# Optimization experiments

Measured on AMD Instinct MI355X. Metric: run time of the kernel, lower is better.

The kernel has to match this reference:

```python
import jax, jax.numpy as jnp
import numpy as np

BN_EPS = 1e-5
LN_EPS = 1e-5


def setup_inputs() -> dict:
    key = jax.random.key(0)
    ks = jax.random.split(key, 8)
    B, D, T = 16, 96, 512  # batch, enc_in (channels), d_model (time/feature)
    H = 2 * T
    residual = jax.random.normal(ks[0], (B, D, T), dtype=jnp.float32)
    # BatchNorm1d(enc_in) affine params
    bn_gamma = jnp.ones((D,), dtype=jnp.float32)
    bn_beta = jnp.zeros((D,), dtype=jnp.float32)
    # LayerNorm(d_model) affine params
    ln_gamma = jnp.ones((T,), dtype=jnp.float32)
    ln_beta = jnp.zeros((T,), dtype=jnp.float32)
    # MLP: Linear(T, 2T) -> GELU -> Linear(2T, T)
    W1 = jax.random.normal(ks[1], (T, H), dtype=jnp.float32) / np.float32(np.sqrt(T))
    b1 = jnp.zeros((H,), dtype=jnp.float32)
    W2 = jax.random.normal(ks[2], (H, T), dtype=jnp.float32) / np.float32(np.sqrt(H))
    b2 = jnp.zeros((T,), dtype=jnp.float32)
    return {"residual": residual, "bn_gamma": bn_gamma, "bn_beta": bn_beta,
            "ln_gamma": ln_gamma, "ln_beta": ln_beta,
            "W1": W1, "b1": b1, "W2": W2, "b2": b2}


def _var_cor_attention(x):
    # x: [B, D, T]; queries = keys = values = x
    B, D, T = x.shape
    f = jnp.fft.rfft(x, axis=-1)                       # [B, D, F]
    # pairwise spectral product q_i * conj(k_j): [B, D, D, F]
    res = f[:, :, None, :] * jnp.conj(f[:, None, :, :])
    corr = jnp.fft.irfft(res, axis=-1).mean(axis=-1)   # [B, D, D]
    scale = np.float32(1.0 / np.sqrt(T))
    corr = jax.nn.softmax(corr * scale, axis=-1)
    V = jnp.einsum('bsd,bde->bse', corr, x)            # [B, D, T]
    return V


def reference(residual, bn_gamma, bn_beta, ln_gamma, ln_beta, W1, b1, W2, b2):
    # attention + residual
    x = _var_cor_attention(residual) + residual        # [B, D, T]
    # BatchNorm1d over channel dim D: stats over (B, T), biased variance
    mu = x.mean(axis=(0, 2), keepdims=True)
    var = ((x - mu) ** 2).mean(axis=(0, 2), keepdims=True)
    x = (x - mu) * jax.lax.rsqrt(var + BN_EPS)
    x = x * bn_gamma[None, :, None] + bn_beta[None, :, None]
    # MLP (exact GELU, torch default) + residual
    h = jax.nn.gelu(jnp.einsum('bdt,th->bdh', x, W1) + b1, approximate=False)
    y = jnp.einsum('bdh,ht->bdt', h, W2) + b2 + x
    # LayerNorm over last dim T
    mu2 = y.mean(axis=-1, keepdims=True)
    var2 = ((y - mu2) ** 2).mean(axis=-1, keepdims=True)
    y = (y - mu2) * jax.lax.rsqrt(var2 + LN_EPS)
    return y * ln_gamma + ln_beta
```

## Files before the change

kernel.cpp:

```cpp
#include <hip/hip_runtime.h>
#include <math.h>
#include <stdint.h>

#define BB 16
#define DD 96
#define TT 512
#define HH 1024
#define NROW (BB*DD)
#define KT2 (HH/32)

typedef __attribute__((ext_vector_type(4))) float floatx4;
typedef __attribute__((ext_vector_type(8))) short short8;

#define WSOFF_X     0u
#define WSOFF_A     3145728u
#define WSOFF_HFRAG WSOFF_A
#define WSOFF_W1BF  6291456u
#define WSOFF_W2BF  7340032u
#define WSOFF_PS    8388608u
#define WSOFF_PS2   8437760u
#define WSOFF_SCSH  8486912u

__device__ __forceinline__ uint16_t f2bf(float v) {
    uint32_t u = __float_as_uint(v);
    uint32_t r = 0x7fffu + ((u >> 16) & 1u);
    return (uint16_t)((u + r) >> 16);
}

__global__ __launch_bounds__(256) void k_pre(const float* __restrict__ residual,
                                             const float* __restrict__ W1,
                                             const float* __restrict__ W2,
                                             float* __restrict__ A,
                                             uint16_t* __restrict__ w1bf,
                                             uint16_t* __restrict__ w2bf) {
    __shared__ float sl[DD];
    const int bid = blockIdx.x;
    const int tid = threadIdx.x;
    const int wave = tid >> 6;
    const int lane = tid & 63;
    const int q = lane >> 4, l15 = lane & 15;

    if (bid < BB) {
        #pragma unroll
        for (int rr = 0; rr < 24; ++rr) {
            int i = wave*24 + rr;
            const float* p = residual + ((size_t)bid*DD + i)*TT;
            float acc = 0.f;
            #pragma unroll
            for (int u = 0; u < TT/64; ++u) acc += p[lane + u*64];
            #pragma unroll
            for (int o = 32; o > 0; o >>= 1) acc += __shfl_down(acc, o, 64);
            if (lane == 0) sl[i] = acc;
        }
        __syncthreads();
        if (tid < DD) {
            const float c = 1.0f / (512.0f * 22.627416997969522f);
            float si = sl[tid] * c;
            float m = -1e30f;
            for (int j = 0; j < DD; ++j) m = fmaxf(m, si * sl[j]);
            float sum = 0.f;
            for (int j = 0; j < DD; ++j) sum += __expf(si * sl[j] - m);
            float inv = 1.0f / sum;
            float* Ao = A + ((size_t)bid*DD + tid)*DD;
            for (int j = 0; j < DD; ++j) Ao[j] = __expf(si * sl[j] - m) * inv;
        }
    } else {
        int wgid = (bid - BB)*4 + wave;
        const int nw = (512 - BB)*4;
        for (int u = wgid; u < 2048; u += nw) {
            const float* W; uint16_t* ob; int KT, N, b;
            if (u < 1024) { W = W1; ob = w1bf; KT = 16; N = 1024; b = u; }
            else          { W = W2; ob = w2bf; KT = 32; N = 512;  b = u - 1024; }
            int tile_n = b / KT, tile_k = b % KT;
            const float* src = W + (size_t)(tile_k*32 + q*8)*N + tile_n*16 + l15;
            uint16_t tmp[8];
            #pragma unroll
            for (int j = 0; j < 8; ++j) tmp[j] = f2bf(src[(size_t)j*N]);
            uint16_t* dst = ob + ((size_t)b*64 + lane)*8;
            *reinterpret_cast<ushort4*>(dst)     = *reinterpret_cast<ushort4*>(&tmp[0]);
            *reinterpret_cast<ushort4*>(dst + 4) = *reinterpret_cast<ushort4*>(&tmp[4]);
        }
    }
}

__global__ __launch_bounds__(256) void k_attn(const float* __restrict__ residual,
                                              const float* __restrict__ A,
                                              float* __restrict__ x,
                                              float* __restrict__ ps,
                                              float* __restrict__ ps2) {
    __shared__ float rlds[DD*64];
    const int u = blockIdx.x;
    const int b = u >> 5, chunk = (u >> 2) & 7, ig = u & 3;
    const int tid = threadIdx.x;
    const int wave = tid >> 6;
    const int lane = tid & 63;

    const float4* rb4 = reinterpret_cast<const float4*>(residual + (size_t)b*DD*TT);
    float4* rl4 = reinterpret_cast<float4*>(rlds);
    #pragma unroll
    for (int s = 0; s < 6; ++s) {
        int idx = tid + s*256;
        int i = idx >> 4, t4 = idx & 15;
        rl4[idx] = rb4[(size_t)i*(TT/4) + chunk*16 + t4];
    }
    __syncthreads();

    int i0 = ig*24 + wave*6;
    const float* Ab = A + ((size_t)b*DD + i0)*DD;
    float acc[6];
    #pragma unroll
    for (int rr = 0; rr < 6; ++rr) acc[rr] = rlds[(i0+rr)*64 + lane];
    #pragma unroll 4
    for (int j4 = 0; j4 < DD/4; ++j4) {
        float4 a[6];
        #pragma unroll
        for (int rr = 0; rr < 6; ++rr)
            a[rr] = *reinterpret_cast<const float4*>(Ab + rr*DD + j4*4);
        float rv[4];
        #pragma unroll
        for (int uu = 0; uu < 4; ++uu) rv[uu] = rlds[(j4*4+uu)*64 + lane];
        #pragma unroll
        for (int rr = 0; rr < 6; ++rr) {
            acc[rr] = fmaf(a[rr].x, rv[0], acc[rr]);
            acc[rr] = fmaf(a[rr].y, rv[1], acc[rr]);
            acc[rr] = fmaf(a[rr].z, rv[2], acc[rr]);
            acc[rr] = fmaf(a[rr].w, rv[3], acc[rr]);
        }
    }
    #pragma unroll
    for (int rr = 0; rr < 6; ++rr) {
        float v = acc[rr];
        x[((size_t)b*DD + i0 + rr)*TT + chunk*64 + lane] = v;
        float s1 = v, s2 = v*v;
        #pragma unroll
        for (int o = 32; o > 0; o >>= 1) {
            s1 += __shfl_down(s1, o, 64);
            s2 += __shfl_down(s2, o, 64);
        }
        if (lane == 0) {
            int d = i0 + rr;
            ps [d*128 + b*8 + chunk] = s1;
            ps2[d*128 + b*8 + chunk] = s2;
        }
    }
}

__global__ __launch_bounds__(256) void k_gemm1(const float* __restrict__ x,
                                               const float* __restrict__ ps,
                                               const float* __restrict__ ps2,
                                               const float* __restrict__ bng,
                                               const float* __restrict__ bnb,
                                               const uint16_t* __restrict__ w1bf,
                                               const float* __restrict__ b1,
                                               uint16_t* __restrict__ hfrag,
                                               float* __restrict__ scsh) {
    __shared__ __align__(16) char SM[27136];
    uint16_t* fragA = (uint16_t*)SM;
    uint16_t* cs    = (uint16_t*)(SM + 16384);
    float*    fin   = (float*)(SM + 24832);
    float*    scs   = (float*)(SM + 26368);
    const int bid = blockIdx.x;
    const int tid = threadIdx.x;
    const int wave = tid >> 6;
    const int lane = tid & 63;
    const int q = lane >> 4, l15 = lane & 15;

    if (tid < 192) {
        int d = tid >> 1, h = tid & 1;
        const float4* p1 = reinterpret_cast<const float4*>(ps  + d*128 + h*64);
        const float4* p2 = reinterpret_cast<const float4*>(ps2 + d*128 + h*64);
        float a1 = 0.f, a2 = 0.f;
        #pragma unroll
        for (int j = 0; j < 16; ++j) {
            float4 v = p1[j]; a1 += v.x+v.y+v.z+v.w;
            float4 w = p2[j]; a2 += w.x+w.y+w.z+w.w;
        }
        fin[tid*2]   = a1;
        fin[tid*2+1] = a2;
    }
    __syncthreads();
    if (tid < DD) {
        float s1 = fin[tid*4]   + fin[tid*4+2];
        float s2 = fin[tid*4+1] + fin[tid*4+3];
        const float invn = 1.0f / (float)(BB*TT);
        float mu  = s1 * invn;
        float var = s2 * invn - mu*mu;
        float rs  = rsqrtf(var + 1e-5f);
        float scv = rs * bng[tid];
        float shv = bnb[tid] - mu*scv;
        scs[tid]      = scv;
        scs[DD + tid] = shv;
        if (bid == 0) { scsh[tid] = scv; scsh[DD + tid] = shv; }
    }
    __syncthreads();

    const int mtile = bid >> 2, nq = bid & 3;
    #pragma unroll
    for (int r4 = 0; r4 < 4; ++r4) {
        int pi = tid + r4*256;
        int kk = pi >> 6, pl = pi & 63;
        int pq = pl >> 4, pr = pl & 15;
        int row = mtile*16 + pr;
        int d = row % DD;
        float scv = scs[d], shv = scs[DD + d];
        const float* xp = x + (size_t)row*TT + kk*32 + pq*8;
        float4 v0 = *reinterpret_cast<const float4*>(xp);
        float4 v1 = *reinterpret_cast<const float4*>(xp + 4);
        ushort4 o0, o1;
        o0.x = f2bf(v0.x*scv + shv); o0.y = f2bf(v0.y*scv + shv);
        o0.z = f2bf(v0.z*scv + shv); o0.w = f2bf(v0.w*scv + shv);
        o1.x = f2bf(v1.x*scv + shv); o1.y = f2bf(v1.y*scv + shv);
        o1.z = f2bf(v1.z*scv + shv); o1.w = f2bf(v1.w*scv + shv);
        uint16_t* fp = fragA + ((size_t)kk*64 + pl)*8;
        *reinterpret_cast<ushort4*>(fp)     = o0;
        *reinterpret_cast<ushort4*>(fp + 4) = o1;
    }
    __syncthreads();

    int n0 = nq*256 + wave*64;
    floatx4 acc4[4] = {};
    #pragma unroll
    for (int kk = 0; kk < 16; ++kk) {
        short8 a = *reinterpret_cast<const short8*>(fragA + (kk*64 + lane)*8);
        #pragma unroll
        for (int nf = 0; nf < 4; ++nf) {
            int ct = (n0 >> 4) + nf;
            short8 bfr = *reinterpret_cast<const short8*>(
                w1bf + ((size_t)(ct*16 + kk)*64 + lane)*8);
            acc4[nf] = __builtin_amdgcn_mfma_f32_16x16x32_bf16(a, bfr, acc4[nf], 0, 0, 0);
        }
    }
    #pragma unroll
    for (int nf = 0; nf < 4; ++nf) {
        int coll = wave*64 + nf*16 + l15;
        float bias = b1[nq*256 + coll];
        #pragma unroll
        for (int r = 0; r < 4; ++r) {
            float v = acc4[nf][r] + bias;
            float gl = 0.5f * v * (1.0f + erff(v * 0.7071067811865475f));
            cs[(q*4 + r)*264 + coll] = f2bf(gl);
        }
    }
    __syncthreads();
    #pragma unroll
    for (int cc = 0; cc < 2; ++cc) {
        int c = wave*2 + cc;
        const uint4* srcp = reinterpret_cast<const uint4*>(cs + l15*264 + c*32 + q*8);
        size_t chunk = (size_t)mtile*KT2 + nq*8 + c;
        reinterpret_cast<uint4*>(hfrag)[chunk*64 + lane] = *srcp;
    }
}

__global__ __launch_bounds__(256) void k_gemm2(const uint16_t* __restrict__ hfrag,
                                               const uint16_t* __restrict__ w2bf,
                                               const float* __restrict__ b2,
                                               const float* __restrict__ x,
                                               const float* __restrict__ scsh,
                                               const float* __restrict__ lng,
                                               const float* __restrict__ lnb,
                                               float* __restrict__ out) {
    __shared__ float lnred[128];
    const int mtile = blockIdx.x;
    const int tid = threadIdx.x;
    const int wave = tid >> 6;
    const int lane = tid & 63;
    const int q = lane >> 4, l15 = lane & 15;
    const int m0 = mtile*16;
    const int n0 = wave*128;

    floatx4 acc[8] = {};
    const uint16_t* ap = hfrag + ((size_t)mtile*KT2*64 + lane)*8;
    #pragma unroll
    for (int kk = 0; kk < 32; ++kk) {
        short8 a = *reinterpret_cast<const short8*>(ap + kk*512);
        #pragma unroll
        for (int nf = 0; nf < 8; ++nf) {
            int ct = (n0 >> 4) + nf;
            short8 bfr = *reinterpret_cast<const short8*>(
                w2bf + ((size_t)(ct*32 + kk)*64 + lane)*8);
            acc[nf] = __builtin_amdgcn_mfma_f32_16x16x32_bf16(a, bfr, acc[nf], 0, 0, 0);
        }
    }
    float s_pt[4]  = {0.f,0.f,0.f,0.f};
    float s2_pt[4] = {0.f,0.f,0.f,0.f};
    #pragma unroll
    for (int r = 0; r < 4; ++r) {
        int row = m0 + q*4 + r;
        int d = row % DD;
        float scv = scsh[d], shv = scsh[DD + d];
        #pragma unroll
        for (int nf = 0; nf < 8; ++nf) {
            int col = n0 + nf*16 + l15;
            float v = acc[nf][r] + b2[col] + x[(size_t)row*TT + col]*scv + shv;
            acc[nf][r] = v;
            s_pt[r]  += v;
            s2_pt[r] += v*v;
        }
    }
    #pragma unroll
    for (int o = 1; o < 16; o <<= 1) {
        #pragma unroll
        for (int r = 0; r < 4; ++r) {
            s_pt[r]  += __shfl_xor(s_pt[r],  o, 64);
            s2_pt[r] += __shfl_xor(s2_pt[r], o, 64);
        }
    }
    if (l15 == 0) {
        #pragma unroll
        for (int r = 0; r < 4; ++r) {
            lnred[(wave*16 + q*4 + r)*2]     = s_pt[r];
            lnred[(wave*16 + q*4 + r)*2 + 1] = s2_pt[r];
        }
    }
    __syncthreads();
    #pragma unroll
    for (int r = 0; r < 4; ++r) {
        int rloc = q*4 + r;
        float s1 = lnred[rloc*2]   + lnred[(16+rloc)*2]   + lnred[(32+rloc)*2]   + lnred[(48+rloc)*2];
        float s2 = lnred[rloc*2+1] + lnred[(16+rloc)*2+1] + lnred[(32+rloc)*2+1] + lnred[(48+rloc)*2+1];
        const float invT = 1.0f / (float)TT;
        float mu  = s1 * invT;
        float var = s2 * invT - mu*mu;
        float rs  = rsqrtf(var + 1e-5f);
        int row = m0 + rloc;
        #pragma unroll
        for (int nf = 0; nf < 8; ++nf) {
            int col = n0 + nf*16 + l15;
            out[(size_t)row*TT + col] = (acc[nf][r] - mu)*rs*lng[col] + lnb[col];
        }
    }
}

extern "C" void kernel_launch(void* const* d_in, const int* in_sizes, int n_in,
                              void* d_out, int out_size, void* d_ws, size_t ws_size,
                              hipStream_t stream) {
    (void)in_sizes; (void)n_in; (void)out_size; (void)ws_size;
    const float* residual = (const float*)d_in[0];
    const float* bng = (const float*)d_in[1];
    const float* bnb = (const float*)d_in[2];
    const float* lng = (const float*)d_in[3];
    const float* lnb = (const float*)d_in[4];
    const float* W1  = (const float*)d_in[5];
    const float* b1  = (const float*)d_in[6];
    const float* W2  = (const float*)d_in[7];
    const float* b2  = (const float*)d_in[8];
    float* out = (float*)d_out;
    char* ws = (char*)d_ws;
    float*    x     = (float*)(ws + WSOFF_X);
    float*    A     = (float*)(ws + WSOFF_A);
    uint16_t* hfrag = (uint16_t*)(ws + WSOFF_HFRAG);
    uint16_t* w1bf  = (uint16_t*)(ws + WSOFF_W1BF);
    uint16_t* w2bf  = (uint16_t*)(ws + WSOFF_W2BF);
    float*    ps    = (float*)(ws + WSOFF_PS);
    float*    ps2   = (float*)(ws + WSOFF_PS2);
    float*    scsh  = (float*)(ws + WSOFF_SCSH);

    k_pre  <<<512, 256, 0, stream>>>(residual, W1, W2, A, w1bf, w2bf);
    k_attn <<<512, 256, 0, stream>>>(residual, A, x, ps, ps2);
    k_gemm1<<<384, 256, 0, stream>>>(x, ps, ps2, bng, bnb, w1bf, b1, hfrag, scsh);
    k_gemm2<<<96, 256, 0, stream>>>(hfrag, w2bf, b2, x, scsh, lng, lnb, out);
}
```

Before: 134.0 us.

## Spread GEMM column work across more waves per block and stage A in LDS

k_gemm1 now runs 8 waves per block (512 threads), each computing 32 output columns instead of 64. k_gemm2 runs 16 waves per block (1024 threads), each computing 32 columns, with the shared 16-row A fragment staged once into LDS rather than read from global by every wave. The LayerNorm partial-sum reduction is widened to 16 waves. The aim is more latency-hiding waves and less per-wave serial MFMA work in these small-grid GEMMs, at the cost of higher register and LDS pressure per block and an extra barrier.

```diff
diff --git a/kernel.cpp b/kernel.cpp
--- a/kernel.cpp
+++ b/kernel.cpp
@@ -145,7 +145,7 @@
     }
 }
 
-__global__ __launch_bounds__(256) void k_gemm1(const float* __restrict__ x,
+__global__ __launch_bounds__(512) void k_gemm1(const float* __restrict__ x,
                                                const float* __restrict__ ps,
                                                const float* __restrict__ ps2,
                                                const float* __restrict__ bng,
@@ -159,7 +159,8 @@
     uint16_t* cs    = (uint16_t*)(SM + 16384);
     float*    fin   = (float*)(SM + 24832);
     float*    scs   = (float*)(SM + 26368);
-    const int bid = blockIdx.x;
+    const int mtile = blockIdx.x;
+    const int nq    = blockIdx.y;
     const int tid = threadIdx.x;
     const int wave = tid >> 6;
     const int lane = tid & 63;
@@ -190,14 +191,13 @@
         float shv = bnb[tid] - mu*scv;
         scs[tid]      = scv;
         scs[DD + tid] = shv;
-        if (bid == 0) { scsh[tid] = scv; scsh[DD + tid] = shv; }
-    }
-    __syncthreads();
-
-    const int mtile = bid >> 2, nq = bid & 3;
-    #pragma unroll
-    for (int r4 = 0; r4 < 4; ++r4) {
-        int pi = tid + r4*256;
+        if (mtile == 0 && nq == 0) { scsh[tid] = scv; scsh[DD + tid] = shv; }
+    }
+    __syncthreads();
+
+    #pragma unroll
+    for (int r4 = 0; r4 < 2; ++r4) {
+        int pi = tid + r4*512;
         int kk = pi >> 6, pl = pi & 63;
         int pq = pl >> 4, pr = pl & 15;
         int row = mtile*16 + pr;
@@ -217,13 +217,13 @@
     }
     __syncthreads();
 
-    int n0 = nq*256 + wave*64;
-    floatx4 acc4[4] = {};
+    const int n0 = nq*256 + wave*32;
+    floatx4 acc4[2] = {};
     #pragma unroll
     for (int kk = 0; kk < 16; ++kk) {
         short8 a = *reinterpret_cast<const short8*>(fragA + (kk*64 + lane)*8);
         #pragma unroll
-        for (int nf = 0; nf < 4; ++nf) {
+        for (int nf = 0; nf < 2; ++nf) {
             int ct = (n0 >> 4) + nf;
             short8 bfr = *reinterpret_cast<const short8*>(
                 w1bf + ((size_t)(ct*16 + kk)*64 + lane)*8);
@@ -231,8 +231,8 @@
         }
     }
     #pragma unroll
-    for (int nf = 0; nf < 4; ++nf) {
-        int coll = wave*64 + nf*16 + l15;
+    for (int nf = 0; nf < 2; ++nf) {
+        int coll = wave*32 + nf*16 + l15;
         float bias = b1[nq*256 + coll];
         #pragma unroll
         for (int r = 0; r < 4; ++r) {
@@ -242,39 +242,47 @@
         }
     }
     __syncthreads();
-    #pragma unroll
-    for (int cc = 0; cc < 2; ++cc) {
-        int c = wave*2 + cc;
+    {
+        int c = wave;
         const uint4* srcp = reinterpret_cast<const uint4*>(cs + l15*264 + c*32 + q*8);
         size_t chunk = (size_t)mtile*KT2 + nq*8 + c;
         reinterpret_cast<uint4*>(hfrag)[chunk*64 + lane] = *srcp;
     }
 }
 
-__global__ __launch_bounds__(256) void k_gemm2(const uint16_t* __restrict__ hfrag,
-                                               const uint16_t* __restrict__ w2bf,
-                                               const float* __restrict__ b2,
-                                               const float* __restrict__ x,
-                                               const float* __restrict__ scsh,
-                                               const float* __restrict__ lng,
-                                               const float* __restrict__ lnb,
-                                               float* __restrict__ out) {
-    __shared__ float lnred[128];
+__global__ __launch_bounds__(1024) void k_gemm2(const uint16_t* __restrict__ hfrag,
+                                                const uint16_t* __restrict__ w2bf,
+                                                const float* __restrict__ b2,
+                                                const float* __restrict__ x,
+                                                const float* __restrict__ scsh,
+                                                const float* __restrict__ lng,
+                                                const float* __restrict__ lnb,
+                                                float* __restrict__ out) {
+    __shared__ __align__(16) char SM2[32768 + 2048];
+    uint16_t* aLDS  = (uint16_t*)SM2;
+    float*    lnred = (float*)(SM2 + 32768);
     const int mtile = blockIdx.x;
     const int tid = threadIdx.x;
     const int wave = tid >> 6;
     const int lane = tid & 63;
     const int q = lane >> 4, l15 = lane & 15;
     const int m0 = mtile*16;
-    const int n0 = wave*128;
-
-    floatx4 acc[8] = {};
-    const uint16_t* ap = hfrag + ((size_t)mtile*KT2*64 + lane)*8;
+    const int n0 = wave*32;
+
+    {
+        const uint4* hsrc = reinterpret_cast<const uint4*>(hfrag + (size_t)mtile*KT2*64*8);
+        uint4* adst = reinterpret_cast<uint4*>(aLDS);
+        adst[tid]        = hsrc[tid];
+        adst[tid + 1024] = hsrc[tid + 1024];
+    }
+    __syncthreads();
+
+    floatx4 acc[2] = {};
     #pragma unroll
     for (int kk = 0; kk < 32; ++kk) {
-        short8 a = *reinterpret_cast<const short8*>(ap + kk*512);
-        #pragma unroll
-        for (int nf = 0; nf < 8; ++nf) {
+        short8 a = *reinterpret_cast<const short8*>(aLDS + (kk*64 + lane)*8);
+        #pragma unroll
+        for (int nf = 0; nf < 2; ++nf) {
             int ct = (n0 >> 4) + nf;
             short8 bfr = *reinterpret_cast<const short8*>(
                 w2bf + ((size_t)(ct*32 + kk)*64 + lane)*8);
@@ -289,7 +297,7 @@
         int d = row % DD;
         float scv = scsh[d], shv = scsh[DD + d];
         #pragma unroll
-        for (int nf = 0; nf < 8; ++nf) {
+        for (int nf = 0; nf < 2; ++nf) {
             int col = n0 + nf*16 + l15;
             float v = acc[nf][r] + b2[col] + x[(size_t)row*TT + col]*scv + shv;
             acc[nf][r] = v;
@@ -316,15 +324,19 @@
     #pragma unroll
     for (int r = 0; r < 4; ++r) {
         int rloc = q*4 + r;
-        float s1 = lnred[rloc*2]   + lnred[(16+rloc)*2]   + lnred[(32+rloc)*2]   + lnred[(48+rloc)*2];
-        float s2 = lnred[rloc*2+1] + lnred[(16+rloc)*2+1] + lnred[(32+rloc)*2+1] + lnred[(48+rloc)*2+1];
+        float s1 = 0.f, s2 = 0.f;
+        #pragma unroll
+        for (int w = 0; w < 16; ++w) {
+            s1 += lnred[(w*16 + rloc)*2];
+            s2 += lnred[(w*16 + rloc)*2 + 1];
+        }
         const float invT = 1.0f / (float)TT;
         float mu  = s1 * invT;
         float var = s2 * invT - mu*mu;
         float rs  = rsqrtf(var + 1e-5f);
         int row = m0 + rloc;
         #pragma unroll
-        for (int nf = 0; nf < 8; ++nf) {
+        for (int nf = 0; nf < 2; ++nf) {
             int col = n0 + nf*16 + l15;
             out[(size_t)row*TT + col] = (acc[nf][r] - mu)*rs*lng[col] + lnb[col];
         }
@@ -357,6 +369,6 @@
 
     k_pre  <<<512, 256, 0, stream>>>(residual, W1, W2, A, w1bf, w2bf);
     k_attn <<<512, 256, 0, stream>>>(residual, A, x, ps, ps2);
-    k_gemm1<<<384, 256, 0, stream>>>(x, ps, ps2, bng, bnb, w1bf, b1, hfrag, scsh);
-    k_gemm2<<<96, 256, 0, stream>>>(hfrag, w2bf, b2, x, scsh, lng, lnb, out);
-}
+    k_gemm1<<<dim3(96, 4), 512, 0, stream>>>(x, ps, ps2, bng, bnb, w1bf, b1, hfrag, scsh);
+    k_gemm2<<<96, 1024, 0, stream>>>(hfrag, w2bf, b2, x, scsh, lng, lnb, out);
+}
```

After: 131.4 us. Within noise of the previous version (-1.9%).
